# Kernel optimization log

Measured on AMD Instinct MI355X. Metric: run time of the kernel, lower is better.

## Reference

```python
import jax, jax.numpy as jnp
import numpy as np

B, S, D, H, NUM_LABELS = 16, 1024, 1024, 16, 3
LN_EPS = 1e-5


def setup_inputs() -> dict:
    key = jax.random.key(0)
    ks = iter(jax.random.split(key, 16))

    def w(shape, k):
        return jax.random.normal(k, shape, jnp.float32) * 0.02

    inp = {}
    inp["embedded"] = jax.random.normal(next(ks), (B, S, D), jnp.float32)
    inp["attention_mask"] = jnp.ones((B, S), jnp.float32)
    for pfx in ("p2h", "h2p"):
        for name in ("q", "k", "v", "o"):
            inp[f"{pfx}_W{name}"] = w((D, D), next(ks))
            inp[f"{pfx}_b{name}"] = jnp.zeros((D,), jnp.float32)
        inp[f"{pfx}_ln_g"] = jnp.ones((D,), jnp.float32)
        inp[f"{pfx}_ln_b"] = jnp.zeros((D,), jnp.float32)
    inp["W1"] = w((4 * D, D), next(ks)); inp["b1"] = jnp.zeros((D,), jnp.float32)
    inp["W2"] = w((D, D // 2), next(ks)); inp["b2"] = jnp.zeros((D // 2,), jnp.float32)
    inp["W3"] = w((D // 2, NUM_LABELS), next(ks)); inp["b3"] = jnp.zeros((NUM_LABELS,), jnp.float32)
    return inp


def _layernorm(x, g, b):
    mu = jnp.mean(x, axis=-1, keepdims=True)
    var = jnp.mean(jnp.square(x - mu), axis=-1, keepdims=True)
    return (x - mu) / jnp.sqrt(var + LN_EPS) * g + b


def _cross_attn(q_in, kv_in, kv_mask, Wq, bq, Wk, bk, Wv, bv, Wo, bo, g, bln):
    Bs, Sq, Dm = q_in.shape
    Sk = kv_in.shape[1]
    hd = Dm // H
    Q = (q_in @ Wq + bq).reshape(Bs, Sq, H, hd)
    K = (kv_in @ Wk + bk).reshape(Bs, Sk, H, hd)
    V = (kv_in @ Wv + bv).reshape(Bs, Sk, H, hd)
    scores = jnp.einsum("bqhd,bkhd->bhqk", Q, K) / jnp.sqrt(jnp.float32(hd))
    scores = jnp.where(kv_mask[:, None, None, :] == 0, jnp.float32(-1e9), scores)
    wts = jax.nn.softmax(scores, axis=-1)  # dropout is identity in eval
    att = jnp.einsum("bhqk,bkhd->bqhd", wts, V).reshape(Bs, Sq, Dm)
    return _layernorm(att @ Wo + bo + q_in, g, bln)


def _pool(x, m):
    s = jnp.sum(x * m[:, :, None], axis=1)
    d = jnp.clip(jnp.sum(m, axis=1, keepdims=True), 1e-9, None)
    return s / d


def reference(embedded, attention_mask,
              p2h_Wq, p2h_bq, p2h_Wk, p2h_bk, p2h_Wv, p2h_bv, p2h_Wo, p2h_bo, p2h_ln_g, p2h_ln_b,
              h2p_Wq, h2p_bq, h2p_Wk, h2p_bk, h2p_Wv, h2p_bv, h2p_Wo, h2p_bo, h2p_ln_g, h2p_ln_b,
              W1, b1, W2, b2, W3, b3):
    half = embedded.shape[1] // 2
    premise, hypothesis = embedded[:, :half], embedded[:, half:]
    pm, hm = attention_mask[:, :half], attention_mask[:, half:]
    p2h = _cross_attn(premise, hypothesis, hm,
                      p2h_Wq, p2h_bq, p2h_Wk, p2h_bk, p2h_Wv, p2h_bv, p2h_Wo, p2h_bo, p2h_ln_g, p2h_ln_b)
    h2p = _cross_attn(hypothesis, premise, pm,
                      h2p_Wq, h2p_bq, h2p_Wk, h2p_bk, h2p_Wv, h2p_bv, h2p_Wo, h2p_bo, h2p_ln_g, h2p_ln_b)
    feats = jnp.concatenate([_pool(premise, pm), _pool(hypothesis, hm),
                             _pool(p2h, pm), _pool(h2p, hm)], axis=-1)
    h1 = jax.nn.relu(feats @ W1 + b1)
    h2 = jax.nn.relu(h1 @ W2 + b2)
    return h2 @ W3 + b3
```

## Files before the change

### kernel.cpp

```cpp
#include <hip/hip_runtime.h>
#include <hip/hip_bf16.h>

typedef __attribute__((ext_vector_type(8))) __bf16 bf16x8;
typedef __attribute__((ext_vector_type(4))) float f32x4;
typedef __attribute__((ext_vector_type(4))) int i32x4;
typedef __attribute__((ext_vector_type(4))) unsigned short u16x4;

#define MFMA16(a, b, c) __builtin_amdgcn_mfma_f32_16x16x32_bf16((a), (b), (c), 0, 0, 0)

__device__ __forceinline__ void gload_lds16(const void* g, void* l)
{
    __builtin_amdgcn_global_load_lds(
        (const __attribute__((address_space(1))) unsigned int*)g,
        (__attribute__((address_space(3))) unsigned int*)l, 16, 0, 0);
}

__global__ __launch_bounds__(256) void cast_emb_kernel(const float* __restrict__ emb,
                                                       __bf16* __restrict__ Pb,
                                                       __bf16* __restrict__ Hb)
{
    int i = (blockIdx.x * 256 + threadIdx.x) * 4;
    int r = i >> 10, d = i & 1023;
    size_t src = ((size_t)(r >> 9) * 1024 + (r & 511)) * 1024 + d;
    f32x4 p = *(const f32x4*)(emb + src);
    f32x4 h = *(const f32x4*)(emb + src + 512 * 1024);
    union { __bf16 b[4]; u16x4 u; } cp, ch;
#pragma unroll
    for (int j = 0; j < 4; ++j) { cp.b[j] = (__bf16)p[j]; ch.b[j] = (__bf16)h[j]; }
    *(u16x4*)(Pb + i) = cp.u;
    *(u16x4*)(Hb + i) = ch.u;
}

struct WPtrs { const float* p[8]; };
__global__ __launch_bounds__(256) void cast_wt_kernel(WPtrs wp, __bf16* __restrict__ Wt0)
{
    const float* W = wp.p[blockIdx.z];
    __bf16* Wt = Wt0 + (size_t)blockIdx.z * 1048576;
    __shared__ float tile[32][33];
    int n0 = blockIdx.x * 32, k0 = blockIdx.y * 32;
    int tx = threadIdx.x, ty = threadIdx.y;
#pragma unroll
    for (int i = ty; i < 32; i += 8)
        tile[i][tx] = W[(size_t)(k0 + i) * 1024 + n0 + tx];
    __syncthreads();
#pragma unroll
    for (int i = ty; i < 32; i += 8)
        Wt[(size_t)(n0 + i) * 1024 + k0 + tx] = (__bf16)tile[tx][i];
}

template <int EPI>
__global__ __launch_bounds__(256, 2) void gemm_bt(const __bf16* __restrict__ A,
                                                  const __bf16* __restrict__ Bt,
                                                  const float* __restrict__ bias,
                                                  const float* __restrict__ bias2,
                                                  __bf16* __restrict__ Cb,
                                                  __bf16* __restrict__ Cb2,
                                                  float* __restrict__ Cf,
                                                  const float* __restrict__ resid,
                                                  int resid_half, int M, int N, int K)
{
    __shared__ __align__(16) __bf16 As[128 * 32];
    __shared__ __align__(16) __bf16 Bs[128 * 32];
    const int t = threadIdx.x;
    const int l = t & 63, w = t >> 6;
    const int wr = w >> 1, wc = w & 1;
    const int lrow = l & 15, lk = l >> 4;
    const int m0 = blockIdx.y * 128, n0 = blockIdx.x * 128;
    const int r0 = t >> 2, kc0 = (t & 3) * 8;

    const __bf16* gA0 = A + (size_t)(m0 + r0) * K + kc0;
    const __bf16* gA1 = gA0 + (size_t)64 * K;
    const __bf16* gB0 = Bt + (size_t)(n0 + r0) * K + kc0;
    const __bf16* gB1 = gB0 + (size_t)64 * K;
    __bf16* dA0 = &As[r0 * 32 + kc0];
    __bf16* dA1 = &As[(r0 + 64) * 32 + kc0];
    __bf16* dB0 = &Bs[r0 * 32 + kc0];
    __bf16* dB1 = &Bs[(r0 + 64) * 32 + kc0];

    const f32x4 zero = {0.f, 0.f, 0.f, 0.f};
    f32x4 acc[4][4];
#pragma unroll
    for (int mi = 0; mi < 4; ++mi)
#pragma unroll
        for (int ni = 0; ni < 4; ++ni) acc[mi][ni] = zero;

    const int nk = K >> 5;
    for (int kt = 0; kt < nk; ++kt) {
        const int ko = kt * 32;
        gload_lds16(gA0 + ko, dA0);
        gload_lds16(gA1 + ko, dA1);
        gload_lds16(gB0 + ko, dB0);
        gload_lds16(gB1 + ko, dB1);
        __syncthreads();
        bf16x8 af[4], bfv[4];
#pragma unroll
        for (int mi = 0; mi < 4; ++mi)
            af[mi] = *(const bf16x8*)(&As[(wr * 64 + mi * 16 + lrow) * 32 + lk * 8]);
#pragma unroll
        for (int ni = 0; ni < 4; ++ni)
            bfv[ni] = *(const bf16x8*)(&Bs[(wc * 64 + ni * 16 + lrow) * 32 + lk * 8]);
#pragma unroll
        for (int mi = 0; mi < 4; ++mi)
#pragma unroll
            for (int ni = 0; ni < 4; ++ni)
                acc[mi][ni] = MFMA16(af[mi], bfv[ni], acc[mi][ni]);
        __syncthreads();
    }

#pragma unroll
    for (int mi = 0; mi < 4; ++mi) {
#pragma unroll
        for (int ni = 0; ni < 4; ++ni) {
            int col = n0 + wc * 64 + ni * 16 + lrow;
            float bv = (EPI == 3 && col >= 1024) ? bias2[col - 1024] : bias[col];
#pragma unroll
            for (int r = 0; r < 4; ++r) {
                int row = m0 + wr * 64 + mi * 16 + lk * 4 + r;
                float v = acc[mi][ni][r] + bv;
                if (EPI == 0) {
                    Cb[(size_t)row * N + col] = (__bf16)v;
                } else if (EPI == 3) {
                    if (col < 1024) {
                        Cb[(size_t)row * 1024 + col] = (__bf16)v;
                    } else {
                        int c2 = col - 1024;
                        int b_ = row >> 9, pos = row & 511;
                        int h_ = c2 >> 6, hd = c2 & 63;
                        Cb2[(((size_t)(b_ * 16 + h_) * 64 + hd) << 9) + pos] = (__bf16)v;
                    }
                } else {
                    int b_ = row >> 9, s = row & 511;
                    float rv = resid[((size_t)b_ * 1024 + resid_half + s) * 1024 + col];
                    Cf[(size_t)row * N + col] = v + rv;
                }
            }
        }
    }
}

__global__ __launch_bounds__(256, 3) void attn_kernel(const __bf16* __restrict__ Q,
                                                      const __bf16* __restrict__ Kb,
                                                      const __bf16* __restrict__ Vt,
                                                      const float* __restrict__ mask,
                                                      int mask_half,
                                                      __bf16* __restrict__ att)
{
    __shared__ __align__(16) __bf16 KB[2][128 * 64];
    __shared__ __align__(16) __bf16 Pt[64 * 128];
    __shared__ __align__(16) float msk[512];
    const int bh = blockIdx.x, b = bh >> 4, h = bh & 15;
    const int q0 = blockIdx.y * 64;
    const int tid = threadIdx.x, l = tid & 63, w = tid >> 6;
    const int lrow = l & 15, lk = l >> 4;

    const __bf16* kbase = Kb + ((size_t)b * 512) * 1024 + h * 64;
    const __bf16* vsrc = Vt + (size_t)bh * 64 * 512;

    auto stage = [&](int t, int buf) {
        char* dst = (char*)KB[buf];
#pragma unroll
        for (int i = 0; i < 4; ++i) {
            int c = tid + i * 256;
            int pos = c >> 3, gslot = (c & 7) ^ (pos & 7);
            gload_lds16(kbase + (size_t)(t * 128 + pos) * 1024 + gslot * 8, dst + c * 16);
        }
    };

    stage(0, 0);
    for (int i = tid; i < 512; i += 256) msk[i] = mask[b * 1024 + mask_half + i];

    const int qrow = q0 + w * 16 + lrow;
    const __bf16* qptr = Q + ((size_t)(b * 512 + qrow)) * 1024 + h * 64;
    bf16x8 qf0 = *(const bf16x8*)(qptr + lk * 8);
    bf16x8 qf1 = *(const bf16x8*)(qptr + 32 + lk * 8);

    const f32x4 zero = {0.f, 0.f, 0.f, 0.f};
    f32x4 av[4];
#pragma unroll
    for (int ni = 0; ni < 4; ++ni) av[ni] = zero;
    float m_run = -3e38f, su = 0.f;
    const int psw = lrow & 7;
    char* prowp = (char*)Pt + (w * 16 + lrow) * 256;
    f32x4 sc[8];

#pragma unroll
    for (int t = 0; t < 4; ++t) {
        __syncthreads();
        const char* kbuf = (const char*)KB[t & 1];
#pragma unroll
        for (int jj = 0; jj < 8; ++jj) {
            const char* kb = kbuf + (jj * 16 + lrow) * 128;
            bf16x8 k0 = *(const bf16x8*)(kb + ((lk ^ psw) << 4));
            bf16x8 k1 = *(const bf16x8*)(kb + (((lk + 4) ^ psw) << 4));
            f32x4 c = zero;
            c = MFMA16(k0, qf0, c);
            c = MFMA16(k1, qf1, c);
            sc[jj] = c;
        }
        if (t < 3) stage(t + 1, (t + 1) & 1);

        const int koff = t * 128;
        float mt = -3e38f;
#pragma unroll
        for (int jj = 0; jj < 8; ++jj) {
            f32x4 mv = *(const f32x4*)(&msk[koff + jj * 16 + lk * 4]);
#pragma unroll
            for (int r = 0; r < 4; ++r) {
                float s = sc[jj][r] * 0.125f;
                if (mv[r] == 0.f) s = -1e9f;
                sc[jj][r] = s;
                mt = fmaxf(mt, s);
            }
        }
        mt = fmaxf(mt, __shfl_xor(mt, 16));
        mt = fmaxf(mt, __shfl_xor(mt, 32));
        float m_new = fmaxf(m_run, mt);
        float f = __expf(m_run - m_new);
        float s0 = 0.f, s1 = 0.f;
#pragma unroll
        for (int jj = 0; jj < 8; ++jj) {
            float e0 = __expf(sc[jj][0] - m_new);
            float e1 = __expf(sc[jj][1] - m_new);
            float e2 = __expf(sc[jj][2] - m_new);
            float e3 = __expf(sc[jj][3] - m_new);
            sc[jj][0] = e0; sc[jj][1] = e1; sc[jj][2] = e2; sc[jj][3] = e3;
            s0 += e0 + e1;
            s1 += e2 + e3;
        }
        float ssum = s0 + s1;
        ssum += __shfl_xor(ssum, 16);
        ssum += __shfl_xor(ssum, 32);
        su = su * f + ssum;
        m_run = m_new;
#pragma unroll
        for (int r = 0; r < 4; ++r) {
            float fr = __shfl(f, (l & 48) | (lk * 4 + r));
#pragma unroll
            for (int ni = 0; ni < 4; ++ni) av[ni][r] *= fr;
        }

#pragma unroll
        for (int jj = 0; jj < 8; ++jj) {
            union { __bf16 b[4]; unsigned long long u; } pk;
#pragma unroll
            for (int r = 0; r < 4; ++r) pk.b[r] = (__bf16)sc[jj][r];
            int slot2 = jj * 2 + (lk >> 1);
            *(unsigned long long*)(prowp + (((slot2 ^ psw) << 4) | ((lk & 1) << 3))) = pk.u;
        }
#pragma unroll
        for (int ks = 0; ks < 4; ++ks) {
            bf16x8 pf = *(const bf16x8*)(prowp + (((ks * 4 + lk) ^ psw) << 4));
#pragma unroll
            for (int ni = 0; ni < 4; ++ni) {
                bf16x8 vf = *(const bf16x8*)(&vsrc[(ni * 16 + lrow) * 512 + koff + ks * 32 + lk * 8]);
                av[ni] = MFMA16(pf, vf, av[ni]);
            }
        }
    }

    const float inv = 1.f / su;
#pragma unroll
    for (int r = 0; r < 4; ++r) {
        float ivr = __shfl(inv, (l & 48) | (lk * 4 + r));
        int qq = q0 + w * 16 + lk * 4 + r;
#pragma unroll
        for (int ni = 0; ni < 4; ++ni)
            att[((size_t)(b * 512 + qq)) * 1024 + h * 64 + ni * 16 + lrow] =
                (__bf16)(av[ni][r] * ivr);
    }
}

__global__ __launch_bounds__(256) void ln_kernel(const float* __restrict__ X,
                                                 const float* __restrict__ g,
                                                 const float* __restrict__ bta,
                                                 __bf16* __restrict__ out)
{
    const int r = blockIdx.x, t = threadIdx.x;
    const float* x = X + (size_t)r * 1024;
    f32x4 v = *(const f32x4*)(x + t * 4);
    float s = v[0] + v[1] + v[2] + v[3];
    float q = v[0] * v[0] + v[1] * v[1] + v[2] * v[2] + v[3] * v[3];
#pragma unroll
    for (int d = 1; d < 64; d <<= 1) { s += __shfl_xor(s, d); q += __shfl_xor(q, d); }
    __shared__ float rs[4], rq[4];
    if ((t & 63) == 0) { rs[t >> 6] = s; rq[t >> 6] = q; }
    __syncthreads();
    s = rs[0] + rs[1] + rs[2] + rs[3];
    q = rq[0] + rq[1] + rq[2] + rq[3];
    float mu = s * (1.f / 1024.f);
    float var = q * (1.f / 1024.f) - mu * mu;
    float rstd = rsqrtf(var + 1e-5f);
#pragma unroll
    for (int j = 0; j < 4; ++j) {
        int c = t * 4 + j;
        out[(size_t)r * 1024 + c] = (__bf16)((v[j] - mu) * rstd * g[c] + bta[c]);
    }
}

__global__ __launch_bounds__(256) void pool_f32_kernel(const float* __restrict__ X,
                                                       const float* __restrict__ mask,
                                                       float* __restrict__ feats)
{
    const int b = blockIdx.y, d0 = blockIdx.x * 64, half = blockIdx.z * 512;
    const int t = threadIdx.x, d = d0 + (t & 63), sl = t >> 6;
    float acc = 0.f, ms = 0.f;
#pragma unroll 4
    for (int s = sl * 128; s < sl * 128 + 128; ++s) {
        float m = mask[b * 1024 + half + s];
        acc += X[((size_t)b * 1024 + half + s) * 1024 + d] * m;
        ms += m;
    }
    __shared__ float ra[4][64];
    __shared__ float rm[4];
    ra[sl][t & 63] = acc;
    if ((t & 63) == 0) rm[sl] = ms;
    __syncthreads();
    if (t < 64) {
        float a = ra[0][t] + ra[1][t] + ra[2][t] + ra[3][t];
        float m = rm[0] + rm[1] + rm[2] + rm[3];
        feats[b * 4096 + blockIdx.z * 1024 + d0 + t] = a / fmaxf(m, 1e-9f);
    }
}

__global__ __launch_bounds__(256) void pool_bf16_kernel(const __bf16* __restrict__ X,
                                                        const float* __restrict__ mask,
                                                        int half, float* __restrict__ feats,
                                                        int off)
{
    const int b = blockIdx.y, d0 = blockIdx.x * 64;
    const int t = threadIdx.x, d = d0 + (t & 63), sl = t >> 6;
    float acc = 0.f, ms = 0.f;
#pragma unroll 4
    for (int s = sl * 128; s < sl * 128 + 128; ++s) {
        float m = mask[b * 1024 + half + s];
        acc += (float)X[((size_t)b * 512 + s) * 1024 + d] * m;
        ms += m;
    }
    __shared__ float ra[4][64];
    __shared__ float rm[4];
    ra[sl][t & 63] = acc;
    if ((t & 63) == 0) rm[sl] = ms;
    __syncthreads();
    if (t < 64) {
        float a = ra[0][t] + ra[1][t] + ra[2][t] + ra[3][t];
        float m = rm[0] + rm[1] + rm[2] + rm[3];
        feats[b * 4096 + off + d0 + t] = a / fmaxf(m, 1e-9f);
    }
}

__global__ __launch_bounds__(256) void fc_init_kernel(const float* __restrict__ b1,
                                                      const float* __restrict__ b2,
                                                      float* __restrict__ h1,
                                                      float* __restrict__ h2)
{
    int i = blockIdx.x * 256 + threadIdx.x;
    if (i < 16 * 1024) h1[i] = b1[i & 1023];
    else h2[i - 16 * 1024] = b2[(i - 16 * 1024) & 511];
}

template <int CH, int RELU_IN>
__global__ __launch_bounds__(256) void fc_atomic_kernel(const float* __restrict__ in,
                                                        const float* __restrict__ W,
                                                        float* __restrict__ out,
                                                        int IF, int OF)
{
    __shared__ float ins[16 * CH];
    const int t = threadIdx.x;
    const int col = blockIdx.x * 256 + t;
    const int i0 = blockIdx.y * CH;
#pragma unroll
    for (int idx = t; idx < 16 * CH; idx += 256) {
        int b = idx / CH, i = idx % CH;
        float v = in[b * IF + i0 + i];
        if (RELU_IN) v = fmaxf(v, 0.f);
        ins[idx] = v;
    }
    __syncthreads();
    float acc[16];
#pragma unroll
    for (int b = 0; b < 16; ++b) acc[b] = 0.f;
#pragma unroll 4
    for (int i = 0; i < CH; ++i) {
        float wv = W[(size_t)(i0 + i) * OF + col];
#pragma unroll
        for (int b = 0; b < 16; ++b) acc[b] += ins[b * CH + i] * wv;
    }
#pragma unroll
    for (int b = 0; b < 16; ++b) atomicAdd(out + b * OF + col, acc[b]);
}

__global__ __launch_bounds__(64) void mlp3_kernel(const float* __restrict__ h2,
                                                  const float* __restrict__ W3,
                                                  const float* __restrict__ b3,
                                                  float* __restrict__ out)
{
    int b = blockIdx.x, t = threadIdx.x;
    float a0 = 0.f, a1 = 0.f, a2 = 0.f;
    for (int i = t; i < 512; i += 64) {
        float hv = fmaxf(h2[b * 512 + i], 0.f);
        a0 += hv * W3[i * 3 + 0];
        a1 += hv * W3[i * 3 + 1];
        a2 += hv * W3[i * 3 + 2];
    }
#pragma unroll
    for (int d = 1; d < 64; d <<= 1) {
        a0 += __shfl_xor(a0, d);
        a1 += __shfl_xor(a1, d);
        a2 += __shfl_xor(a2, d);
    }
    if (t == 0) {
        out[b * 3 + 0] = a0 + b3[0];
        out[b * 3 + 1] = a1 + b3[1];
        out[b * 3 + 2] = a2 + b3[2];
    }
}

extern "C" void kernel_launch(void* const* d_in, const int* in_sizes, int n_in,
                              void* d_out, int out_size, void* d_ws, size_t ws_size,
                              hipStream_t stream)
{
    const float* emb  = (const float*)d_in[0];
    const float* mask = (const float*)d_in[1];
    const float* W1 = (const float*)d_in[22];
    const float* b1 = (const float*)d_in[23];
    const float* W2 = (const float*)d_in[24];
    const float* b2 = (const float*)d_in[25];
    const float* W3 = (const float*)d_in[26];
    const float* b3 = (const float*)d_in[27];

    char* ws = (char*)d_ws;
    constexpr size_t MB = 1ull << 20;
    __bf16* Pb    = (__bf16*)(ws);
    __bf16* Hb    = (__bf16*)(ws + 16 * MB);
    __bf16* Wt    = (__bf16*)(ws + 32 * MB);
    __bf16* Qb    = (__bf16*)(ws + 48 * MB);
    __bf16* Kb    = (__bf16*)(ws + 64 * MB);
    __bf16* Vt    = (__bf16*)(ws + 80 * MB);
    __bf16* attb  = (__bf16*)(ws + 96 * MB);
    float*  Of    = (float*) (ws + 48 * MB);
    __bf16* ctx   = (__bf16*)(ws + 112 * MB);
    float*  feats = (float*) (ws + 128 * MB);
    float*  h1    = (float*) (ws + 128 * MB + 512 * 1024);
    float*  h2    = (float*) (ws + 129 * MB);

    cast_emb_kernel<<<8192, 256, 0, stream>>>(emb, Pb, Hb);
    WPtrs wp;
    const int widx[8] = {2, 4, 6, 8, 12, 14, 16, 18};
    for (int i = 0; i < 8; ++i) wp.p[i] = (const float*)d_in[widx[i]];
    cast_wt_kernel<<<dim3(32, 32, 8), dim3(32, 8), 0, stream>>>(wp, Wt);

    dim3 gg(8, 64);
    dim3 gkv(16, 64);
    for (int dir = 0; dir < 2; ++dir) {
        const __bf16* qin  = dir ? Hb : Pb;
        const __bf16* kvin = dir ? Pb : Hb;
        const int base = dir ? 12 : 2;
        const __bf16* wq  = Wt + (size_t)(dir * 4 + 0) * 1048576;
        const __bf16* wkv = Wt + (size_t)(dir * 4 + 1) * 1048576;
        const __bf16* wo  = Wt + (size_t)(dir * 4 + 3) * 1048576;
        const float* bq  = (const float*)d_in[base + 1];
        const float* bk  = (const float*)d_in[base + 3];
        const float* bv  = (const float*)d_in[base + 5];
        const float* bo  = (const float*)d_in[base + 7];
        const float* lng = (const float*)d_in[base + 8];
        const float* lnb = (const float*)d_in[base + 9];
        const int kvhalf  = dir ? 0 : 512;
        const int reshalf = dir ? 512 : 0;

        gemm_bt<0><<<gg, 256, 0, stream>>>(qin, wq, bq, nullptr, Qb, nullptr,
                                           nullptr, nullptr, 0, 8192, 1024, 1024);
        gemm_bt<3><<<gkv, 256, 0, stream>>>(kvin, wkv, bk, bv, Kb, Vt,
                                            nullptr, nullptr, 0, 8192, 2048, 1024);
        attn_kernel<<<dim3(256, 8), 256, 0, stream>>>(Qb, Kb, Vt, mask, kvhalf, attb);
        gemm_bt<2><<<gg, 256, 0, stream>>>(attb, wo, bo, nullptr, nullptr, nullptr,
                                           Of, emb, reshalf, 8192, 1024, 1024);
        ln_kernel<<<8192, 256, 0, stream>>>(Of, lng, lnb, ctx);
        pool_bf16_kernel<<<dim3(16, 16), 256, 0, stream>>>(ctx, mask, dir ? 512 : 0,
                                                           feats, 2048 + dir * 1024);
    }
    pool_f32_kernel<<<dim3(16, 16, 2), 256, 0, stream>>>(emb, mask, feats);

    fc_init_kernel<<<96, 256, 0, stream>>>(b1, b2, h1, h2);
    fc_atomic_kernel<128, 0><<<dim3(4, 32), 256, 0, stream>>>(feats, W1, h1, 4096, 1024);
    fc_atomic_kernel<32, 1><<<dim3(2, 32), 256, 0, stream>>>(h1, W2, h2, 1024, 512);
    mlp3_kernel<<<16, 64, 0, stream>>>(h2, W3, b3, (float*)d_out);
}
```

Baseline: 603.4 us.

## Batch both attention directions into single launches per stage

Both cross-attention directions now run in shared launches instead of a per-direction loop. The inputs are packed into one contiguous buffer, and per-direction weights and biases are passed through pointer structs. Each GEMM, the attention, layernorm and pooling stage then runs once over twice the rows, which halves the launch count and doubles the grid size per launch for better GPU fill. The workspace layout is reshuffled so buffers are reused, and the GEMM launch bound rises to 3 blocks per CU, which may add register pressure or spills.

```diff
diff --git a/kernel.cpp b/kernel.cpp
--- a/kernel.cpp
+++ b/kernel.cpp
@@ -15,9 +15,11 @@
         (__attribute__((address_space(3))) unsigned int*)l, 16, 0, 0);
 }
 
+struct GemmW { const __bf16* w[2]; const float* bias[2]; const float* bias2[2]; };
+struct LnW   { const float* g[2]; const float* b[2]; };
+
 __global__ __launch_bounds__(256) void cast_emb_kernel(const float* __restrict__ emb,
-                                                       __bf16* __restrict__ Pb,
-                                                       __bf16* __restrict__ Hb)
+                                                       __bf16* __restrict__ A)
 {
     int i = (blockIdx.x * 256 + threadIdx.x) * 4;
     int r = i >> 10, d = i & 1023;
@@ -27,8 +29,8 @@
     union { __bf16 b[4]; u16x4 u; } cp, ch;
 #pragma unroll
     for (int j = 0; j < 4; ++j) { cp.b[j] = (__bf16)p[j]; ch.b[j] = (__bf16)h[j]; }
-    *(u16x4*)(Pb + i) = cp.u;
-    *(u16x4*)(Hb + i) = ch.u;
+    *(u16x4*)(A + i) = cp.u;
+    *(u16x4*)(A + 8388608 + i) = ch.u;
 }
 
 struct WPtrs { const float* p[8]; };
@@ -49,15 +51,13 @@
 }
 
 template <int EPI>
-__global__ __launch_bounds__(256, 2) void gemm_bt(const __bf16* __restrict__ A,
-                                                  const __bf16* __restrict__ Bt,
-                                                  const float* __restrict__ bias,
-                                                  const float* __restrict__ bias2,
+__global__ __launch_bounds__(256, 3) void gemm_bt(const __bf16* __restrict__ A,
+                                                  GemmW gw,
                                                   __bf16* __restrict__ Cb,
-                                                  __bf16* __restrict__ Cb2,
+                                                  __bf16* __restrict__ Vt,
                                                   float* __restrict__ Cf,
                                                   const float* __restrict__ resid,
-                                                  int resid_half, int M, int N, int K)
+                                                  int K)
 {
     __shared__ __align__(16) __bf16 As[128 * 32];
     __shared__ __align__(16) __bf16 Bs[128 * 32];
@@ -66,9 +66,12 @@
     const int wr = w >> 1, wc = w & 1;
     const int lrow = l & 15, lk = l >> 4;
     const int m0 = blockIdx.y * 128, n0 = blockIdx.x * 128;
+    const int dir = m0 >> 13;
     const int r0 = t >> 2, kc0 = (t & 3) * 8;
 
-    const __bf16* gA0 = A + (size_t)(m0 + r0) * K + kc0;
+    const int am0 = (EPI == 3) ? (m0 ^ 8192) : m0;
+    const __bf16* Bt = gw.w[dir];
+    const __bf16* gA0 = A + (size_t)(am0 + r0) * K + kc0;
     const __bf16* gA1 = gA0 + (size_t)64 * K;
     const __bf16* gB0 = Bt + (size_t)(n0 + r0) * K + kc0;
     const __bf16* gB1 = gB0 + (size_t)64 * K;
@@ -112,26 +115,31 @@
 #pragma unroll
         for (int ni = 0; ni < 4; ++ni) {
             int col = n0 + wc * 64 + ni * 16 + lrow;
-            float bv = (EPI == 3 && col >= 1024) ? bias2[col - 1024] : bias[col];
+            float bv = (EPI == 3 && col >= 1024) ? gw.bias2[dir][col - 1024]
+                                                 : gw.bias[dir][col & 1023];
 #pragma unroll
             for (int r = 0; r < 4; ++r) {
                 int row = m0 + wr * 64 + mi * 16 + lk * 4 + r;
                 float v = acc[mi][ni][r] + bv;
                 if (EPI == 0) {
-                    Cb[(size_t)row * N + col] = (__bf16)v;
+                    Cb[(size_t)row * 1024 + col] = (__bf16)v;
                 } else if (EPI == 3) {
                     if (col < 1024) {
                         Cb[(size_t)row * 1024 + col] = (__bf16)v;
                     } else {
                         int c2 = col - 1024;
-                        int b_ = row >> 9, pos = row & 511;
+                        int local = row & 8191;
+                        int b_ = local >> 9, pos = local & 511;
                         int h_ = c2 >> 6, hd = c2 & 63;
-                        Cb2[(((size_t)(b_ * 16 + h_) * 64 + hd) << 9) + pos] = (__bf16)v;
+                        Vt[(size_t)dir * 8388608 +
+                           (((size_t)(b_ * 16 + h_) * 64 + hd) << 9) + pos] = (__bf16)v;
                     }
                 } else {
-                    int b_ = row >> 9, s = row & 511;
-                    float rv = resid[((size_t)b_ * 1024 + resid_half + s) * 1024 + col];
-                    Cf[(size_t)row * N + col] = v + rv;
+                    int local = row & 8191;
+                    int b_ = local >> 9, s = local & 511;
+                    int rh = dir * 512;
+                    float rv = resid[((size_t)b_ * 1024 + rh + s) * 1024 + col];
+                    Cf[(size_t)row * 1024 + col] = v + rv;
                 }
             }
         }
@@ -142,19 +150,22 @@
                                                       const __bf16* __restrict__ Kb,
                                                       const __bf16* __restrict__ Vt,
                                                       const float* __restrict__ mask,
-                                                      int mask_half,
                                                       __bf16* __restrict__ att)
 {
     __shared__ __align__(16) __bf16 KB[2][128 * 64];
     __shared__ __align__(16) __bf16 Pt[64 * 128];
     __shared__ __align__(16) float msk[512];
-    const int bh = blockIdx.x, b = bh >> 4, h = bh & 15;
+    const int dirbh = blockIdx.x;
+    const int dir = dirbh >> 8, bh = dirbh & 255;
+    const int b = bh >> 4, h = bh & 15;
+    const int mask_half = dir ? 0 : 512;
     const int q0 = blockIdx.y * 64;
     const int tid = threadIdx.x, l = tid & 63, w = tid >> 6;
     const int lrow = l & 15, lk = l >> 4;
-
-    const __bf16* kbase = Kb + ((size_t)b * 512) * 1024 + h * 64;
-    const __bf16* vsrc = Vt + (size_t)bh * 64 * 512;
+    const size_t rowbase = (size_t)dir * 8192 + b * 512;
+
+    const __bf16* kbase = Kb + rowbase * 1024 + h * 64;
+    const __bf16* vsrc = Vt + (size_t)dir * 8388608 + (size_t)bh * 64 * 512;
 
     auto stage = [&](int t, int buf) {
         char* dst = (char*)KB[buf];
@@ -169,8 +180,7 @@
     stage(0, 0);
     for (int i = tid; i < 512; i += 256) msk[i] = mask[b * 1024 + mask_half + i];
 
-    const int qrow = q0 + w * 16 + lrow;
-    const __bf16* qptr = Q + ((size_t)(b * 512 + qrow)) * 1024 + h * 64;
+    const __bf16* qptr = Q + (rowbase + q0 + w * 16 + lrow) * 1024 + h * 64;
     bf16x8 qf0 = *(const bf16x8*)(qptr + lk * 8);
     bf16x8 qf1 = *(const bf16x8*)(qptr + 32 + lk * 8);
 
@@ -262,20 +272,21 @@
 #pragma unroll
     for (int r = 0; r < 4; ++r) {
         float ivr = __shfl(inv, (l & 48) | (lk * 4 + r));
-        int qq = q0 + w * 16 + lk * 4 + r;
+        size_t orow = rowbase + q0 + w * 16 + lk * 4 + r;
 #pragma unroll
         for (int ni = 0; ni < 4; ++ni)
-            att[((size_t)(b * 512 + qq)) * 1024 + h * 64 + ni * 16 + lrow] =
-                (__bf16)(av[ni][r] * ivr);
+            att[orow * 1024 + h * 64 + ni * 16 + lrow] = (__bf16)(av[ni][r] * ivr);
     }
 }
 
 __global__ __launch_bounds__(256) void ln_kernel(const float* __restrict__ X,
-                                                 const float* __restrict__ g,
-                                                 const float* __restrict__ bta,
+                                                 LnW lw,
                                                  __bf16* __restrict__ out)
 {
     const int r = blockIdx.x, t = threadIdx.x;
+    const int dir = r >> 13;
+    const float* g = lw.g[dir];
+    const float* bta = lw.b[dir];
     const float* x = X + (size_t)r * 1024;
     f32x4 v = *(const f32x4*)(x + t * 4);
     float s = v[0] + v[1] + v[2] + v[3];
@@ -324,16 +335,16 @@
 
 __global__ __launch_bounds__(256) void pool_bf16_kernel(const __bf16* __restrict__ X,
                                                         const float* __restrict__ mask,
-                                                        int half, float* __restrict__ feats,
-                                                        int off)
-{
-    const int b = blockIdx.y, d0 = blockIdx.x * 64;
+                                                        float* __restrict__ feats)
+{
+    const int b = blockIdx.y, d0 = blockIdx.x * 64, dir = blockIdx.z;
+    const int half = dir * 512;
     const int t = threadIdx.x, d = d0 + (t & 63), sl = t >> 6;
     float acc = 0.f, ms = 0.f;
 #pragma unroll 4
     for (int s = sl * 128; s < sl * 128 + 128; ++s) {
         float m = mask[b * 1024 + half + s];
-        acc += (float)X[((size_t)b * 512 + s) * 1024 + d] * m;
+        acc += (float)X[((size_t)dir * 8192 + b * 512 + s) * 1024 + d] * m;
         ms += m;
     }
     __shared__ float ra[4][64];
@@ -344,7 +355,7 @@
     if (t < 64) {
         float a = ra[0][t] + ra[1][t] + ra[2][t] + ra[3][t];
         float m = rm[0] + rm[1] + rm[2] + rm[3];
-        feats[b * 4096 + off + d0 + t] = a / fmaxf(m, 1e-9f);
+        feats[b * 4096 + 2048 + dir * 1024 + d0 + t] = a / fmaxf(m, 1e-9f);
     }
 }
 
@@ -430,54 +441,47 @@
 
     char* ws = (char*)d_ws;
     constexpr size_t MB = 1ull << 20;
-    __bf16* Pb    = (__bf16*)(ws);
-    __bf16* Hb    = (__bf16*)(ws + 16 * MB);
+    __bf16* A     = (__bf16*)(ws);
     __bf16* Wt    = (__bf16*)(ws + 32 * MB);
     __bf16* Qb    = (__bf16*)(ws + 48 * MB);
-    __bf16* Kb    = (__bf16*)(ws + 64 * MB);
-    __bf16* Vt    = (__bf16*)(ws + 80 * MB);
-    __bf16* attb  = (__bf16*)(ws + 96 * MB);
+    __bf16* Kb    = (__bf16*)(ws + 80 * MB);
+    __bf16* Vt    = (__bf16*)(ws + 112 * MB);
+    __bf16* attb  = (__bf16*)(ws);
     float*  Of    = (float*) (ws + 48 * MB);
-    __bf16* ctx   = (__bf16*)(ws + 112 * MB);
-    float*  feats = (float*) (ws + 128 * MB);
-    float*  h1    = (float*) (ws + 128 * MB + 512 * 1024);
-    float*  h2    = (float*) (ws + 129 * MB);
-
-    cast_emb_kernel<<<8192, 256, 0, stream>>>(emb, Pb, Hb);
+    __bf16* ctx   = (__bf16*)(ws);
+    float*  feats = (float*) (ws + 144 * MB);
+    float*  h1    = (float*) (ws + 144 * MB + 512 * 1024);
+    float*  h2    = (float*) (ws + 145 * MB);
+
+    cast_emb_kernel<<<8192, 256, 0, stream>>>(emb, A);
     WPtrs wp;
     const int widx[8] = {2, 4, 6, 8, 12, 14, 16, 18};
     for (int i = 0; i < 8; ++i) wp.p[i] = (const float*)d_in[widx[i]];
     cast_wt_kernel<<<dim3(32, 32, 8), dim3(32, 8), 0, stream>>>(wp, Wt);
 
-    dim3 gg(8, 64);
-    dim3 gkv(16, 64);
+    GemmW gq, gkv, go;
+    LnW lw;
     for (int dir = 0; dir < 2; ++dir) {
-        const __bf16* qin  = dir ? Hb : Pb;
-        const __bf16* kvin = dir ? Pb : Hb;
         const int base = dir ? 12 : 2;
-        const __bf16* wq  = Wt + (size_t)(dir * 4 + 0) * 1048576;
-        const __bf16* wkv = Wt + (size_t)(dir * 4 + 1) * 1048576;
-        const __bf16* wo  = Wt + (size_t)(dir * 4 + 3) * 1048576;
-        const float* bq  = (const float*)d_in[base + 1];
-        const float* bk  = (const float*)d_in[base + 3];
-        const float* bv  = (const float*)d_in[base + 5];
-        const float* bo  = (const float*)d_in[base + 7];
-        const float* lng = (const float*)d_in[base + 8];
-        const float* lnb = (const float*)d_in[base + 9];
-        const int kvhalf  = dir ? 0 : 512;
-        const int reshalf = dir ? 512 : 0;
-
-        gemm_bt<0><<<gg, 256, 0, stream>>>(qin, wq, bq, nullptr, Qb, nullptr,
-                                           nullptr, nullptr, 0, 8192, 1024, 1024);
-        gemm_bt<3><<<gkv, 256, 0, stream>>>(kvin, wkv, bk, bv, Kb, Vt,
-                                            nullptr, nullptr, 0, 8192, 2048, 1024);
-        attn_kernel<<<dim3(256, 8), 256, 0, stream>>>(Qb, Kb, Vt, mask, kvhalf, attb);
-        gemm_bt<2><<<gg, 256, 0, stream>>>(attb, wo, bo, nullptr, nullptr, nullptr,
-                                           Of, emb, reshalf, 8192, 1024, 1024);
-        ln_kernel<<<8192, 256, 0, stream>>>(Of, lng, lnb, ctx);
-        pool_bf16_kernel<<<dim3(16, 16), 256, 0, stream>>>(ctx, mask, dir ? 512 : 0,
-                                                           feats, 2048 + dir * 1024);
-    }
+        gq.w[dir]  = Wt + (size_t)(dir * 4 + 0) * 1048576;
+        gq.bias[dir]  = (const float*)d_in[base + 1];
+        gq.bias2[dir] = nullptr;
+        gkv.w[dir] = Wt + (size_t)(dir * 4 + 1) * 1048576;
+        gkv.bias[dir]  = (const float*)d_in[base + 3];
+        gkv.bias2[dir] = (const float*)d_in[base + 5];
+        go.w[dir]  = Wt + (size_t)(dir * 4 + 3) * 1048576;
+        go.bias[dir]  = (const float*)d_in[base + 7];
+        go.bias2[dir] = nullptr;
+        lw.g[dir] = (const float*)d_in[base + 8];
+        lw.b[dir] = (const float*)d_in[base + 9];
+    }
+
+    gemm_bt<0><<<dim3(8, 128), 256, 0, stream>>>(A, gq, Qb, nullptr, nullptr, nullptr, 1024);
+    gemm_bt<3><<<dim3(16, 128), 256, 0, stream>>>(A, gkv, Kb, Vt, nullptr, nullptr, 1024);
+    attn_kernel<<<dim3(512, 8), 256, 0, stream>>>(Qb, Kb, Vt, mask, attb);
+    gemm_bt<2><<<dim3(8, 128), 256, 0, stream>>>(attb, go, nullptr, nullptr, Of, emb, 1024);
+    ln_kernel<<<16384, 256, 0, stream>>>(Of, lw, ctx);
+    pool_bf16_kernel<<<dim3(16, 16, 2), 256, 0, stream>>>(ctx, mask, feats);
     pool_f32_kernel<<<dim3(16, 16, 2), 256, 0, stream>>>(emb, mask, feats);
 
     fc_init_kernel<<<96, 256, 0, stream>>>(b1, b2, h1, h2);
```

Result: faster. 569.2 us (-5.7%).
